# Optimization experiments

Measured on AMD Instinct MI355X. Metric: run time of the kernel, lower is better.

The kernel has to match this reference:

```python
import jax, jax.numpy as jnp
import numpy as np

B, T, D = 2, 2048, 2048
NH, NKV = 16, 4
HD = D // NH  # 128
BASE, TSL = 10000.0, 1024


def rotary_tables(T, hd, base=BASE, tsl=TSL):
    # Matches Rotary.forward with rd == hd (rd=0 in __init__ -> full head dim).
    ar = jnp.arange(0, hd, 2, dtype=jnp.float32) / hd
    if T <= tsl:
        inv = 1.0 / (base ** ar)
    else:
        # NTK-style rescale; note right-assoc exponent in original torch code:
        # 1/(base * (T/tsl) ** ((rd/(rd-2)) ** ar))
        inv = 1.0 / (base * jnp.power(T / tsl, jnp.power(hd / (hd - 2.0), ar)))
    f = jnp.outer(jnp.arange(T, dtype=jnp.float32), inv)  # [T, hd//2]
    cos = jnp.cos(f)[None, :, None, :]  # [1,T,1,hd//2]
    sin = jnp.sin(f)[None, :, None, :]
    return cos, sin


def apply_rope(x, cos, sin):
    # full-dim rope: split halves, rotate
    h = x.shape[-1] // 2
    x1, x2 = x[..., :h], x[..., h:]
    return jnp.concatenate((x1 * cos + x2 * sin, -x1 * sin + x2 * cos), axis=-1)


def rms_norm(x):
    eps = jnp.finfo(x.dtype).eps
    return x * jax.lax.rsqrt(jnp.mean(x * x, axis=-1, keepdims=True) + eps)


def setup_inputs() -> dict:
    key = jax.random.key(0)
    k0, k1, k2, k3, k4 = jax.random.split(key, 5)
    s = 0.02
    return {
        "x": jax.random.normal(k0, (B, T, D), jnp.float32),
        "qw": jax.random.normal(k1, (NH * HD, D), jnp.float32) * s,
        "kw": jax.random.normal(k2, (NKV * HD, D), jnp.float32) * s,
        "vw": jax.random.normal(k3, (NKV * HD, D), jnp.float32) * s,
        "ow": jax.random.normal(k4, (D, D), jnp.float32) * s,
        "qg": jnp.ones((NH,), jnp.float32),
    }


def reference(x, qw, kw, vw, ow, qg):
    Bx, Tx, Dx = x.shape
    q = (x @ qw.T).reshape(Bx, Tx, NH, HD)
    k = (x @ kw.T).reshape(Bx, Tx, NKV, HD)
    v = (x @ vw.T).reshape(Bx, Tx, NKV, HD)
    q = rms_norm(q)
    k = rms_norm(k)
    cos, sin = rotary_tables(Tx, HD)
    q = apply_rope(q, cos, sin) * qg[None, None, :, None]
    k = apply_rope(k, cos, sin)
    # GQA: repeat kv heads
    r = NH // NKV
    k = jnp.repeat(k, r, axis=2)  # [B,T,NH,HD]
    v = jnp.repeat(v, r, axis=2)
    scale = 1.0 / jnp.sqrt(jnp.asarray(HD, q.dtype))
    scores = jnp.einsum("bqhd,bkhd->bhqk", q, k) * scale  # [B,NH,T,T]
    causal = jnp.tril(jnp.ones((Tx, Tx), dtype=bool))
    scores = jnp.where(causal[None, None, :, :], scores, jnp.asarray(-jnp.inf, scores.dtype))
    attn = jax.nn.softmax(scores, axis=-1)
    y = jnp.einsum("bhqk,bkhd->bqhd", attn, v)  # [B,T,NH,HD]
    return y.reshape(Bx, Tx, Dx) @ ow.T
```

## Files before the change

### kernel.cpp

```cpp
#include <hip/hip_runtime.h>
#include <hip/hip_bf16.h>
#include <stdint.h>


typedef __attribute__((ext_vector_type(8))) short short8;
typedef __attribute__((ext_vector_type(4))) float f32x4;
typedef __attribute__((ext_vector_type(16))) float f32x16;

#define GLOAD16(gp, lp) \
  __builtin_amdgcn_global_load_lds((const __attribute__((address_space(1))) void*)(gp), \
                                   (__attribute__((address_space(3))) void*)(lp), 16, 0, 0)

#define BAR() do { asm volatile("" ::: "memory"); __builtin_amdgcn_s_barrier(); asm volatile("" ::: "memory"); } while (0)

__device__ __forceinline__ float bf2f(unsigned short u) {
  union { unsigned int i; float f; } v; v.i = ((unsigned int)u) << 16; return v.f;
}
__device__ __forceinline__ unsigned short f2bf(float f) {
  union { float fl; unsigned int i; } v; v.fl = f;
  unsigned int r = v.i + 0x7fffu + ((v.i >> 16) & 1u);
  return (unsigned short)(r >> 16);
}
__device__ __forceinline__ unsigned pk2(float a, float b) {
  return (unsigned)f2bf(a) | ((unsigned)f2bf(b) << 16);
}

__global__ __launch_bounds__(256) void prep_kernel(
    const float* __restrict__ x, const float* __restrict__ qw,
    const float* __restrict__ kw, const float* __restrict__ vw,
    const float* __restrict__ ow,
    unsigned short* __restrict__ xb, unsigned short* __restrict__ wqkv,
    unsigned short* __restrict__ owb, float* __restrict__ cost, float* __restrict__ sint) {
  const int NX = 2097152;
  const int NW = 1572864;
  const int NO = 1048576;
  const int NT = 131072;
  int tid = blockIdx.x * 256 + threadIdx.x;
  if (tid < NX) {
    float4 v = ((const float4*)x)[tid];
    uint2 o; o.x = pk2(v.x, v.y); o.y = pk2(v.z, v.w);
    ((uint2*)xb)[tid] = o;
  } else if (tid < NX + NW) {
    int i = tid - NX; int e = i * 4;
    const float* src = (e < 4194304) ? (qw + e)
                     : (e < 5242880) ? (kw + (e - 4194304))
                                     : (vw + (e - 5242880));
    float4 v = *(const float4*)src;
    uint2 o; o.x = pk2(v.x, v.y); o.y = pk2(v.z, v.w);
    ((uint2*)wqkv)[i] = o;
  } else if (tid < NX + NW + NO) {
    int i = tid - NX - NW;
    float4 v = ((const float4*)ow)[i];
    uint2 o; o.x = pk2(v.x, v.y); o.y = pk2(v.z, v.w);
    ((uint2*)owb)[i] = o;
  } else if (tid < NX + NW + NO + NT) {
    int i = tid - NX - NW - NO;
    int t = i >> 6, j = i & 63;
    float e = exp2f(0.02272008f * (float)j * (1.0f / 64.0f));
    float inv = 1.0f / (10000.0f * exp2f(e));
    float f = (float)t * inv;
    cost[i] = cosf(f);
    sint[i] = sinf(f);
  }
}

template <int IM, int OUTF>
__global__ __launch_bounds__(512) void gemm8ph(const unsigned short* __restrict__ A,
                                               const unsigned short* __restrict__ Bw,
                                               void* __restrict__ Cp,
                                               int MT, int NTn, int N, int K) {
  extern __shared__ char smc[];
  constexpr int S = IM * 8;
  constexpr int IQ = IM / 2;
  constexpr int ASZ = IM * 2048;
  constexpr int DB = 2 * ASZ + 32768;
  constexpr int AL = (IM * 128) / 512;
  const int tid = threadIdx.x;
  const int l = tid & 63, w = tid >> 6;
  const int lane_r = l & 15, lane_g = l >> 4;
  const int wr = w >> 2, wc = w & 3;

  int qch = (MT * NTn) >> 3;
  int orig = blockIdx.x;
  int wgid = (orig & 7) * qch + (orig >> 3);
  int by = wgid / NTn, bx = wgid - by * NTn;
  const int m0 = by * IM * 32, n0 = bx * 256;

  f32x4 acc[IM][4];
#pragma unroll
  for (int i = 0; i < IM; ++i)
#pragma unroll
    for (int j = 0; j < 4; ++j) acc[i][j] = {0.f, 0.f, 0.f, 0.f};

  const unsigned short* srcA[AL]; int ldA[AL];
#pragma unroll
  for (int t = 0; t < AL; ++t) {
    int idx = t * 512 + tid;
    int rc = idx >> 3, kc = idx & 7;
    int wrp = rc >= S ? 1 : 0, rr = rc & (S - 1);
    int row = wrp * 2 * S + rr;
    srcA[t] = A + (size_t)(m0 + row) * K + (kc ^ (rc & 7)) * 8;
    ldA[t] = idx * 16;
  }
  const unsigned short* srcB[2]; int ldB[2];
#pragma unroll
  for (int t = 0; t < 2; ++t) {
    int idx = t * 512 + tid;
    int rc = idx >> 3, kc = idx & 7;
    int nrow = (rc >> 5) * 64 + (rc & 31);
    srcB[t] = Bw + (size_t)(n0 + nrow) * K + (kc ^ (rc & 7)) * 8;
    ldB[t] = idx * 16;
  }
  const int SK = S * K, JK = 32 * K;

  auto STA = [&](int kt, int ih, int dqb) {
    char* d = smc + dqb + ih * ASZ;
#pragma unroll
    for (int t = 0; t < AL; ++t) GLOAD16(srcA[t] + kt + ih * SK, d + ldA[t]);
  };
  auto STB = [&](int kt, int jh, int dqb) {
    char* d = smc + dqb + 2 * ASZ + jh * 16384;
#pragma unroll
    for (int t = 0; t < 2; ++t) GLOAD16(srcB[t] + kt + jh * JK, d + ldB[t]);
  };

  int oA[IQ][2], oB[2][2];
#pragma unroll
  for (int iq = 0; iq < IQ; ++iq)
#pragma unroll
    for (int ks = 0; ks < 2; ++ks) {
      int rc = wr * S + iq * 16 + lane_r;
      oA[iq][ks] = rc * 128 + ((ks * 64 + lane_g * 16) ^ ((rc & 7) << 4));
    }
#pragma unroll
  for (int jj = 0; jj < 2; ++jj)
#pragma unroll
    for (int ks = 0; ks < 2; ++ks) {
      int rc = wc * 32 + jj * 16 + lane_r;
      oB[jj][ks] = rc * 128 + ((ks * 64 + lane_g * 16) ^ ((rc & 7) << 4));
    }

#define VMC() do { if constexpr (IM == 8) asm volatile("s_waitcnt vmcnt(6)" ::: "memory"); \
                   else                   asm volatile("s_waitcnt vmcnt(5)" ::: "memory"); } while (0)
#define VM0() asm volatile("s_waitcnt vmcnt(0)" ::: "memory")
#define MM(IH, JH, BR) do { \
    __builtin_amdgcn_s_setprio(1); \
    _Pragma("unroll") \
    for (int iq = 0; iq < IQ; ++iq) \
      _Pragma("unroll") \
      for (int jj = 0; jj < 2; ++jj) \
        _Pragma("unroll") \
        for (int ks = 0; ks < 2; ++ks) \
          acc[(IH) * IQ + iq][(JH) * 2 + jj] = __builtin_amdgcn_mfma_f32_16x16x32_bf16( \
              af[iq][ks], BR[jj][ks], acc[(IH) * IQ + iq][(JH) * 2 + jj], 0, 0, 0); \
    __builtin_amdgcn_s_setprio(0); } while (0)

  const int NS = K >> 6;
  STA(0, 0, 0); STB(0, 0, 0); STB(0, 1, 0); STA(0, 1, 0);
  STA(64, 0, DB); STB(64, 0, DB); STB(64, 1, DB);
  VMC();
  BAR();

#pragma unroll 1
  for (int s = 0; s < NS; ++s) {
    const int dq = (s & 1) * DB, dn = DB - dq;
    const char* Ab = smc + dq;
    const char* Bb = Ab + 2 * ASZ;
    short8 af[IQ][2], b0[2][2], b1[2][2];
    if (s + 1 < NS) STA((s + 1) << 6, 1, dn);
#pragma unroll
    for (int iq = 0; iq < IQ; ++iq)
#pragma unroll
      for (int ks = 0; ks < 2; ++ks) af[iq][ks] = *(const short8*)(Ab + oA[iq][ks]);
#pragma unroll
    for (int jj = 0; jj < 2; ++jj)
#pragma unroll
      for (int ks = 0; ks < 2; ++ks) b0[jj][ks] = *(const short8*)(Bb + oB[jj][ks]);
    MM(0, 0, b0);
    BAR();
    if (s + 2 < NS) STA((s + 2) << 6, 0, dq);
#pragma unroll
    for (int jj = 0; jj < 2; ++jj)
#pragma unroll
      for (int ks = 0; ks < 2; ++ks) b1[jj][ks] = *(const short8*)(Bb + 16384 + oB[jj][ks]);
    MM(0, 1, b1);
    BAR();
    if (s + 2 < NS) STB((s + 2) << 6, 0, dq);
#pragma unroll
    for (int iq = 0; iq < IQ; ++iq)
#pragma unroll
      for (int ks = 0; ks < 2; ++ks) af[iq][ks] = *(const short8*)(Ab + ASZ + oA[iq][ks]);
    MM(1, 0, b0);
    BAR();
    if (s + 2 < NS) STB((s + 2) << 6, 1, dq);
    MM(1, 1, b1);
    if (s + 2 < NS) VMC(); else VM0();
    BAR();
  }
#undef VMC
#undef VM0
#undef MM

#pragma unroll
  for (int ih = 0; ih < 2; ++ih)
#pragma unroll
    for (int iq = 0; iq < IQ; ++iq) {
      int row = m0 + wr * 2 * S + ih * S + iq * 16 + lane_g * 4;
#pragma unroll
      for (int j = 0; j < 4; ++j) {
        int col = n0 + wc * 64 + j * 16 + lane_r;
#pragma unroll
        for (int r = 0; r < 4; ++r) {
          float v = acc[ih * IQ + iq][j][r];
          if (OUTF)
            ((float*)Cp)[(size_t)(row + r) * N + col] = v;
          else
            ((unsigned short*)Cp)[(size_t)(row + r) * N + col] = f2bf(v);
        }
      }
    }
}

__global__ __launch_bounds__(256) void normrope_kernel(unsigned short* __restrict__ qkv,
                                                       const float* __restrict__ cost,
                                                       const float* __restrict__ sint,
                                                       const float* __restrict__ qg) {
  const int tid = threadIdx.x, l = tid & 63, w = tid >> 6;
  int row = blockIdx.x * 4 + w;
  int tok = row / 20, hh = row - tok * 20;
  int t = tok & 2047;
  bool isq = hh < 16;
  int col0 = isq ? hh * 128 : 2048 + (hh - 16) * 128;
  unsigned short* p = qkv + (size_t)tok * 3072 + col0 + 2 * l;
  unsigned int u = *(const unsigned int*)p;
  float x0 = bf2f((unsigned short)(u & 0xffffu));
  float x1 = bf2f((unsigned short)(u >> 16));
  float ss = x0 * x0 + x1 * x1;
#pragma unroll
  for (int m = 1; m < 64; m <<= 1) ss += __shfl_xor(ss, m);
  float rn = rsqrtf(ss * (1.0f / 128.0f) + 1.1920928955078125e-07f);
  float n0 = x0 * rn, n1 = x1 * rn;
  float p0 = __shfl_xor(n0, 32);
  float p1 = __shfl_xor(n1, 32);
  int jj = (2 * l) & 63;
  float c0 = cost[t * 64 + jj], c1 = cost[t * 64 + jj + 1];
  float s0 = sint[t * 64 + jj], s1 = sint[t * 64 + jj + 1];
  float o0, o1;
  if (l < 32) { o0 = n0 * c0 + p0 * s0; o1 = n1 * c1 + p1 * s1; }
  else        { o0 = -p0 * s0 + n0 * c0; o1 = -p1 * s1 + n1 * c1; }
  if (isq) { float g = qg[hh] * 0.08838834764831845f * 1.4426950408889634f; o0 *= g; o1 *= g; }
  *(unsigned int*)p = pk2(o0, o1);
}

__global__ __launch_bounds__(256) void vtrans_kernel(const unsigned short* __restrict__ qkv,
                                                     unsigned short* __restrict__ vtg) {
  __shared__ unsigned short tile[64][132];
  int bid = blockIdx.x;
  int pan = bid & 7, tt = bid >> 3;
  int b = pan >> 2, kvh = pan & 3;
  int t0 = tt * 64;
  const unsigned short* src = qkv + ((size_t)(b * 2048 + t0)) * 3072 + 2560 + kvh * 128;
#pragma unroll
  for (int i = 0; i < 8; ++i) {
    int idx = i * 256 + threadIdx.x;
    int row = idx >> 5, c4 = idx & 31;
    uint2 v = *(const uint2*)(src + (size_t)row * 3072 + c4 * 4);
    *(uint2*)&tile[row][c4 * 4] = v;
  }
  __syncthreads();
  unsigned short* dst = vtg + (size_t)pan * 262144 + t0;
#pragma unroll
  for (int i = 0; i < 8; ++i) {
    int idx = i * 256 + threadIdx.x;
    int d = idx >> 4, tc = idx & 15;
    unsigned short a0 = tile[tc * 4 + 0][d], a1 = tile[tc * 4 + 1][d];
    unsigned short a2 = tile[tc * 4 + 2][d], a3 = tile[tc * 4 + 3][d];
    uint2 o; o.x = (unsigned)a0 | ((unsigned)a1 << 16);
    o.y = (unsigned)a2 | ((unsigned)a3 << 16);
    *(uint2*)(dst + (size_t)d * 2048 + tc * 4) = o;
  }
}

__global__ __launch_bounds__(256, 2) void attn_fa5(const unsigned short* __restrict__ qkv,
                                                   const unsigned short* __restrict__ vtg,
                                                   unsigned short* __restrict__ y) {
  extern __shared__ char smc[];
  const int tid = threadIdx.x;
  const int l = tid & 63, w = tid >> 6;
  const int lq = l & 31, hi = l >> 5;

  int n = blockIdx.x;
  int pan = n & 7;
  int b = pan >> 2, kvh = pan & 3;
  int idx2 = n >> 3;
  int h = kvh * 4 + (idx2 & 3);
  int pairIdx = idx2 >> 2;
  const size_t rowbase = (size_t)b * 2048;
  const unsigned short* kvK = qkv + rowbase * 3072;
  const unsigned short* vtp = vtg + (size_t)pan * 262144;

  int kg[4], vg[4], sl[4];
#pragma unroll
  for (int t = 0; t < 4; ++t) {
    int idx = t * 256 + tid;
    { int row = idx >> 4, c = idx & 15, gc = c ^ (row & 7);
      kg[t] = row * 3072 + 2048 + kvh * 128 + gc * 8; }
    { int d = idx >> 3, c = idx & 7, gc = c ^ (d & 7);
      vg[t] = d * 2048 + gc * 8; }
    sl[t] = idx * 16;
  }
  const int swq = (lq & 7) << 4;
  int oxd[8];
#pragma unroll
  for (int ds = 0; ds < 8; ++ds) oxd[ds] = (ds * 32 + hi * 16) ^ swq;
  const int krow = lq * 256;
  const int vrow = lq * 128;
  const int pbase = 65536 + w * 4096;
  const int prow = pbase + lq * 128;
  int opw[2][4];
#pragma unroll
  for (int t = 0; t < 2; ++t)
#pragma unroll
    for (int m = 0; m < 4; ++m) opw[t][m] = prow + ((t * 64 + m * 16 + hi * 8) ^ swq);

  auto STAGE = [&](int tile, int bufsel) {
    const unsigned short* srcK = kvK + (size_t)tile * 64 * 3072;
    const unsigned short* srcV = vtp + tile * 64;
    char* kd = smc + bufsel * 16384;
    char* vd = smc + 32768 + bufsel * 16384;
#pragma unroll
    for (int t = 0; t < 4; ++t) {
      GLOAD16(srcK + kg[t], kd + sl[t]);
      GLOAD16(srcV + vg[t], vd + sl[t]);
    }
  };

#pragma unroll 1
  for (int phase = 0; phase < 2; ++phase) {
    const int qt = phase ? pairIdx : 15 - pairIdx;
    const int q0 = qt * 128;
    const int nkb = 2 * qt + 2;
    const int wrow0 = q0 + w * 32;
    const int qrow = wrow0 + lq;

    STAGE(0, 0);
    short8 qf[8];
#pragma unroll
    for (int ds = 0; ds < 8; ++ds)
      qf[ds] = *(const short8*)(qkv + (rowbase + qrow) * 3072 + h * 128 + ds * 16 + hi * 8);

    f32x16 acc[4];
#pragma unroll
    for (int dt = 0; dt < 4; ++dt)
#pragma unroll
      for (int jj = 0; jj < 16; ++jj) acc[dt][jj] = 0.f;
    float mrun = -1e30f, lrun = 0.f;

    __syncthreads();

#pragma unroll 1
    for (int kb = 0; kb < nkb; ++kb) {
      const int cur = kb & 1;
      if (kb + 1 < nkb) STAGE(kb + 1, cur ^ 1);
      const int j0 = kb * 64;
      if (j0 <= wrow0 + 31) {
        const int kbb = cur * 16384;
        const int vbb = 32768 + cur * 16384;
        f32x16 s0, s1;
#pragma unroll
        for (int jj = 0; jj < 16; ++jj) { s0[jj] = 0.f; s1[jj] = 0.f; }
        __builtin_amdgcn_s_setprio(1);
#pragma unroll
        for (int ds = 0; ds < 8; ++ds) {
          short8 kf = *(const short8*)(smc + kbb + krow + oxd[ds]);
          s0 = __builtin_amdgcn_mfma_f32_32x32x16_bf16(kf, qf[ds], s0, 0, 0, 0);
        }
#pragma unroll
        for (int ds = 0; ds < 8; ++ds) {
          short8 kf = *(const short8*)(smc + kbb + 8192 + krow + oxd[ds]);
          s1 = __builtin_amdgcn_mfma_f32_32x32x16_bf16(kf, qf[ds], s1, 0, 0, 0);
        }
        __builtin_amdgcn_s_setprio(0);
        const int rq = qrow - j0;
        if (j0 + 63 > wrow0) {
#pragma unroll
          for (int jj = 0; jj < 16; ++jj) {
            int kl = (jj & 3) + 8 * (jj >> 2) + 4 * hi;
            s0[jj] = (kl > rq) ? -1e30f : s0[jj];
            s1[jj] = (kl + 32 > rq) ? -1e30f : s1[jj];
          }
        }
        float pmax = s0[0];
#pragma unroll
        for (int jj = 0; jj < 16; ++jj) pmax = fmaxf(pmax, fmaxf(s0[jj], s1[jj]));
        pmax = fmaxf(pmax, __shfl_xor(pmax, 32));
        if (!__all(pmax - mrun <= 11.5f)) {
          float mn = fmaxf(mrun, pmax);
          float corr = exp2f(mrun - mn);
          lrun *= corr;
#pragma unroll
          for (int dt = 0; dt < 4; ++dt)
#pragma unroll
            for (int jj = 0; jj < 16; ++jj) acc[dt][jj] *= corr;
          mrun = mn;
        }
        float rs = 0.f;
#pragma unroll
        for (int jj = 0; jj < 16; ++jj) {
          s0[jj] = exp2f(s0[jj] - mrun); rs += s0[jj];
          s1[jj] = exp2f(s1[jj] - mrun); rs += s1[jj];
        }
        rs += __shfl_xor(rs, 32);
        lrun += rs;
#pragma unroll
        for (int m = 0; m < 4; ++m) {
          uint2 p0, p1;
          p0.x = pk2(s0[4 * m], s0[4 * m + 1]); p0.y = pk2(s0[4 * m + 2], s0[4 * m + 3]);
          p1.x = pk2(s1[4 * m], s1[4 * m + 1]); p1.y = pk2(s1[4 * m + 2], s1[4 * m + 3]);
          *(uint2*)(smc + opw[0][m]) = p0;
          *(uint2*)(smc + opw[1][m]) = p1;
        }
        short8 pfr[4];
#pragma unroll
        for (int ksl = 0; ksl < 4; ++ksl)
          pfr[ksl] = *(const short8*)(smc + prow + oxd[ksl]);
        __builtin_amdgcn_s_setprio(1);
#pragma unroll
        for (int ksl = 0; ksl < 4; ++ksl)
#pragma unroll
          for (int dt = 0; dt < 4; ++dt) {
            short8 vf = *(const short8*)(smc + vbb + dt * 4096 + vrow + oxd[ksl]);
            acc[dt] = __builtin_amdgcn_mfma_f32_32x32x16_bf16(vf, pfr[ksl], acc[dt], 0, 0, 0);
          }
        __builtin_amdgcn_s_setprio(0);
      }
      __syncthreads();
    }
    float linv = 1.0f / lrun;
    unsigned short* yrow = y + (rowbase + qrow) * 2048 + h * 128;
#pragma unroll
    for (int dt = 0; dt < 4; ++dt)
#pragma unroll
      for (int m = 0; m < 4; ++m) {
        uint2 o;
        o.x = pk2(acc[dt][4 * m] * linv, acc[dt][4 * m + 1] * linv);
        o.y = pk2(acc[dt][4 * m + 2] * linv, acc[dt][4 * m + 3] * linv);
        *(uint2*)(yrow + dt * 32 + m * 8 + hi * 4) = o;
      }
  }
}

extern "C" void kernel_launch(void* const* d_in, const int* in_sizes, int n_in,
                              void* d_out, int out_size, void* d_ws, size_t ws_size,
                              hipStream_t stream) {
  (void)in_sizes; (void)n_in; (void)out_size; (void)ws_size;
  const float* x  = (const float*)d_in[0];
  const float* qw = (const float*)d_in[1];
  const float* kw = (const float*)d_in[2];
  const float* vw = (const float*)d_in[3];
  const float* ow = (const float*)d_in[4];
  const float* qg = (const float*)d_in[5];

  char* ws = (char*)d_ws;
  unsigned short* xb   = (unsigned short*)(ws + 0);
  unsigned short* vtg  = (unsigned short*)(ws + 0);
  unsigned short* wqkv = (unsigned short*)(ws + 16777216);
  unsigned short* owb  = (unsigned short*)(ws + 29360128);
  unsigned short* qkvb = (unsigned short*)(ws + 37748736);
  unsigned short* y    = (unsigned short*)(ws + 62914560);
  float* cost          = (float*)(ws + 79691776);
  float* sint          = (float*)(ws + 80216064);

  prep_kernel<<<18944, 256, 0, stream>>>(x, qw, kw, vw, ow, xb, wqkv, owb, cost, sint);
  gemm8ph<8, 0><<<192, 512, 131072, stream>>>(xb, wqkv, qkvb, 16, 12, 3072, 2048);
  normrope_kernel<<<20480, 256, 0, stream>>>(qkvb, cost, sint, qg);
  vtrans_kernel<<<256, 256, 0, stream>>>(qkvb, vtg);
  attn_fa5<<<256, 256, 81920, stream>>>(qkvb, vtg, y);
  gemm8ph<4, 1><<<256, 512, 98304, stream>>>(y, owb, d_out, 32, 8, 2048, 2048);
}
```

Before: 214.6 us.

## Split each attention KV tile across two wave groups with final softmax merge

```diff
diff --git a/kernel.cpp b/kernel.cpp
--- a/kernel.cpp
+++ b/kernel.cpp
@@ -281,13 +281,14 @@
   }
 }
 
-__global__ __launch_bounds__(256, 2) void attn_fa5(const unsigned short* __restrict__ qkv,
-                                                   const unsigned short* __restrict__ vtg,
-                                                   unsigned short* __restrict__ y) {
+__global__ __launch_bounds__(512) void attn_fa6(const unsigned short* __restrict__ qkv,
+                                                const unsigned short* __restrict__ vtg,
+                                                unsigned short* __restrict__ y) {
   extern __shared__ char smc[];
   const int tid = threadIdx.x;
   const int l = tid & 63, w = tid >> 6;
   const int lq = l & 31, hi = l >> 5;
+  const int g = w & 3, hh = w >> 2;
 
   int n = blockIdx.x;
   int pan = n & 7;
@@ -299,10 +300,10 @@
   const unsigned short* kvK = qkv + rowbase * 3072;
   const unsigned short* vtp = vtg + (size_t)pan * 262144;
 
-  int kg[4], vg[4], sl[4];
-#pragma unroll
-  for (int t = 0; t < 4; ++t) {
-    int idx = t * 256 + tid;
+  int kg[2], vg[2], sl[2];
+#pragma unroll
+  for (int t = 0; t < 2; ++t) {
+    int idx = t * 512 + tid;
     { int row = idx >> 4, c = idx & 15, gc = c ^ (row & 7);
       kg[t] = row * 3072 + 2048 + kvh * 128 + gc * 8; }
     { int d = idx >> 3, c = idx & 7, gc = c ^ (d & 7);
@@ -310,18 +311,25 @@
     sl[t] = idx * 16;
   }
   const int swq = (lq & 7) << 4;
-  int oxd[8];
-#pragma unroll
-  for (int ds = 0; ds < 8; ++ds) oxd[ds] = (ds * 32 + hi * 16) ^ swq;
-  const int krow = lq * 256;
+  const int krow = (hh * 32 + lq) * 256;
+  int oxk[8];
+#pragma unroll
+  for (int ds = 0; ds < 8; ++ds) oxk[ds] = (ds * 32 + hi * 16) ^ swq;
   const int vrow = lq * 128;
-  const int pbase = 65536 + w * 4096;
+  int oxv[2];
+#pragma unroll
+  for (int ksl = 0; ksl < 2; ++ksl) oxv[ksl] = (hh * 64 + ksl * 32 + hi * 16) ^ swq;
+  const int pbase = 65536 + g * 4096;
   const int prow = pbase + lq * 128;
-  int opw[2][4];
-#pragma unroll
-  for (int t = 0; t < 2; ++t)
-#pragma unroll
-    for (int m = 0; m < 4; ++m) opw[t][m] = prow + ((t * 64 + m * 16 + hi * 8) ^ swq);
+  int opw[4];
+#pragma unroll
+  for (int m = 0; m < 4; ++m) opw[m] = prow + ((hh * 64 + m * 16 + hi * 8) ^ swq);
+  int opr[2];
+#pragma unroll
+  for (int ksl = 0; ksl < 2; ++ksl) opr[ksl] = prow + ((hh * 64 + ksl * 32 + hi * 16) ^ swq);
+  const int mab = (g * 64 + l) * 256;
+  const int mlb = 81920 + (g * 64 + l) * 8;
+  const int lsw = (l & 7) << 4;
 
   auto STAGE = [&](int tile, int bufsel) {
     const unsigned short* srcK = kvK + (size_t)tile * 64 * 3072;
@@ -329,7 +337,7 @@
     char* kd = smc + bufsel * 16384;
     char* vd = smc + 32768 + bufsel * 16384;
 #pragma unroll
-    for (int t = 0; t < 4; ++t) {
+    for (int t = 0; t < 2; ++t) {
       GLOAD16(srcK + kg[t], kd + sl[t]);
       GLOAD16(srcV + vg[t], vd + sl[t]);
     }
@@ -340,7 +348,7 @@
     const int qt = phase ? pairIdx : 15 - pairIdx;
     const int q0 = qt * 128;
     const int nkb = 2 * qt + 2;
-    const int wrow0 = q0 + w * 32;
+    const int wrow0 = q0 + g * 32;
     const int qrow = wrow0 + lq;
 
     STAGE(0, 0);
@@ -363,36 +371,30 @@
       const int cur = kb & 1;
       if (kb + 1 < nkb) STAGE(kb + 1, cur ^ 1);
       const int j0 = kb * 64;
-      if (j0 <= wrow0 + 31) {
+      if (j0 + hh * 32 <= wrow0) {
         const int kbb = cur * 16384;
         const int vbb = 32768 + cur * 16384;
-        f32x16 s0, s1;
-#pragma unroll
-        for (int jj = 0; jj < 16; ++jj) { s0[jj] = 0.f; s1[jj] = 0.f; }
+        f32x16 s;
+#pragma unroll
+        for (int jj = 0; jj < 16; ++jj) s[jj] = 0.f;
         __builtin_amdgcn_s_setprio(1);
 #pragma unroll
         for (int ds = 0; ds < 8; ++ds) {
-          short8 kf = *(const short8*)(smc + kbb + krow + oxd[ds]);
-          s0 = __builtin_amdgcn_mfma_f32_32x32x16_bf16(kf, qf[ds], s0, 0, 0, 0);
-        }
-#pragma unroll
-        for (int ds = 0; ds < 8; ++ds) {
-          short8 kf = *(const short8*)(smc + kbb + 8192 + krow + oxd[ds]);
-          s1 = __builtin_amdgcn_mfma_f32_32x32x16_bf16(kf, qf[ds], s1, 0, 0, 0);
+          short8 kf = *(const short8*)(smc + kbb + krow + oxk[ds]);
+          s = __builtin_amdgcn_mfma_f32_32x32x16_bf16(kf, qf[ds], s, 0, 0, 0);
         }
         __builtin_amdgcn_s_setprio(0);
-        const int rq = qrow - j0;
-        if (j0 + 63 > wrow0) {
+        const int rq = qrow - j0 - hh * 32;
+        if (rq < 31) {
 #pragma unroll
           for (int jj = 0; jj < 16; ++jj) {
             int kl = (jj & 3) + 8 * (jj >> 2) + 4 * hi;
-            s0[jj] = (kl > rq) ? -1e30f : s0[jj];
-            s1[jj] = (kl + 32 > rq) ? -1e30f : s1[jj];
+            s[jj] = (kl > rq) ? -1e30f : s[jj];
           }
         }
-        float pmax = s0[0];
-#pragma unroll
-        for (int jj = 0; jj < 16; ++jj) pmax = fmaxf(pmax, fmaxf(s0[jj], s1[jj]));
+        float pmax = s[0];
+#pragma unroll
+        for (int jj = 1; jj < 16; ++jj) pmax = fmaxf(pmax, s[jj]);
         pmax = fmaxf(pmax, __shfl_xor(pmax, 32));
         if (!__all(pmax - mrun <= 11.5f)) {
           float mn = fmaxf(mrun, pmax);
@@ -406,47 +408,71 @@
         }
         float rs = 0.f;
 #pragma unroll
-        for (int jj = 0; jj < 16; ++jj) {
-          s0[jj] = exp2f(s0[jj] - mrun); rs += s0[jj];
-          s1[jj] = exp2f(s1[jj] - mrun); rs += s1[jj];
-        }
+        for (int jj = 0; jj < 16; ++jj) { s[jj] = exp2f(s[jj] - mrun); rs += s[jj]; }
         rs += __shfl_xor(rs, 32);
         lrun += rs;
 #pragma unroll
         for (int m = 0; m < 4; ++m) {
-          uint2 p0, p1;
-          p0.x = pk2(s0[4 * m], s0[4 * m + 1]); p0.y = pk2(s0[4 * m + 2], s0[4 * m + 3]);
-          p1.x = pk2(s1[4 * m], s1[4 * m + 1]); p1.y = pk2(s1[4 * m + 2], s1[4 * m + 3]);
-          *(uint2*)(smc + opw[0][m]) = p0;
-          *(uint2*)(smc + opw[1][m]) = p1;
-        }
-        short8 pfr[4];
-#pragma unroll
-        for (int ksl = 0; ksl < 4; ++ksl)
-          pfr[ksl] = *(const short8*)(smc + prow + oxd[ksl]);
+          uint2 pv;
+          pv.x = pk2(s[4 * m], s[4 * m + 1]);
+          pv.y = pk2(s[4 * m + 2], s[4 * m + 3]);
+          *(uint2*)(smc + opw[m]) = pv;
+        }
+        short8 pfr[2];
+        pfr[0] = *(const short8*)(smc + opr[0]);
+        pfr[1] = *(const short8*)(smc + opr[1]);
         __builtin_amdgcn_s_setprio(1);
 #pragma unroll
-        for (int ksl = 0; ksl < 4; ++ksl)
+        for (int ksl = 0; ksl < 2; ++ksl)
 #pragma unroll
           for (int dt = 0; dt < 4; ++dt) {
-            short8 vf = *(const short8*)(smc + vbb + dt * 4096 + vrow + oxd[ksl]);
+            short8 vf = *(const short8*)(smc + vbb + dt * 4096 + vrow + oxv[ksl]);
             acc[dt] = __builtin_amdgcn_mfma_f32_32x32x16_bf16(vf, pfr[ksl], acc[dt], 0, 0, 0);
           }
         __builtin_amdgcn_s_setprio(0);
       }
       __syncthreads();
     }
-    float linv = 1.0f / lrun;
-    unsigned short* yrow = y + (rowbase + qrow) * 2048 + h * 128;
-#pragma unroll
-    for (int dt = 0; dt < 4; ++dt)
-#pragma unroll
-      for (int m = 0; m < 4; ++m) {
-        uint2 o;
-        o.x = pk2(acc[dt][4 * m] * linv, acc[dt][4 * m + 1] * linv);
-        o.y = pk2(acc[dt][4 * m + 2] * linv, acc[dt][4 * m + 3] * linv);
-        *(uint2*)(yrow + dt * 32 + m * 8 + hi * 4) = o;
-      }
+    if (hh) {
+#pragma unroll
+      for (int dt = 0; dt < 4; ++dt)
+#pragma unroll
+        for (int q4 = 0; q4 < 4; ++q4) {
+          f32x4 v = {acc[dt][4 * q4], acc[dt][4 * q4 + 1], acc[dt][4 * q4 + 2], acc[dt][4 * q4 + 3]};
+          *(f32x4*)(smc + mab + ((dt * 64 + q4 * 16) ^ lsw)) = v;
+        }
+      *(float2*)(smc + mlb) = {mrun, lrun};
+    }
+    __syncthreads();
+    if (!hh) {
+      float2 ml = *(const float2*)(smc + mlb);
+      float mx = fmaxf(mrun, ml.x);
+      float sc0 = exp2f(mrun - mx), sc1 = exp2f(ml.x - mx);
+      lrun = lrun * sc0 + ml.y * sc1;
+#pragma unroll
+      for (int dt = 0; dt < 4; ++dt)
+#pragma unroll
+        for (int q4 = 0; q4 < 4; ++q4) {
+          f32x4 v = *(const f32x4*)(smc + mab + ((dt * 64 + q4 * 16) ^ lsw));
+#pragma unroll
+          for (int r = 0; r < 4; ++r)
+            acc[dt][4 * q4 + r] = acc[dt][4 * q4 + r] * sc0 + v[r] * sc1;
+        }
+    }
+    __syncthreads();
+    if (!hh) {
+      float linv = 1.0f / lrun;
+      unsigned short* yrow = y + (rowbase + qrow) * 2048 + h * 128;
+#pragma unroll
+      for (int dt = 0; dt < 4; ++dt)
+#pragma unroll
+        for (int m = 0; m < 4; ++m) {
+          uint2 o;
+          o.x = pk2(acc[dt][4 * m] * linv, acc[dt][4 * m + 1] * linv);
+          o.y = pk2(acc[dt][4 * m + 2] * linv, acc[dt][4 * m + 3] * linv);
+          *(uint2*)(yrow + dt * 32 + m * 8 + hi * 4) = o;
+        }
+    }
   }
 }
 
@@ -475,6 +501,6 @@
   gemm8ph<8, 0><<<192, 512, 131072, stream>>>(xb, wqkv, qkvb, 16, 12, 3072, 2048);
   normrope_kernel<<<20480, 256, 0, stream>>>(qkvb, cost, sint, qg);
   vtrans_kernel<<<256, 256, 0, stream>>>(qkvb, vtg);
-  attn_fa5<<<256, 256, 81920, stream>>>(qkvb, vtg, y);
+  attn_fa6<<<256, 512, 83968, stream>>>(qkvb, vtg, y);
   gemm8ph<4, 1><<<256, 512, 98304, stream>>>(y, owb, d_out, 32, 8, 2048, 2048);
 }
```

Measured after the change: 199.4 us. -7.1%, faster.
